# Performance work log

Measured on AMD Instinct MI355X. Metric: run time of the kernel, lower is better.

Reference implementation:

```python
import jax, jax.numpy as jnp
import numpy as np

HID = 512
POOL = 4096
NUM_OBJ = 151
NUM_REL = 51
K = 100
GROUPS = 8
EPS_GN = 1e-5


def _lrga(x, w, b):
    # LowRankAttention: x [N,D] -> [N,2K]
    tmp = jax.nn.relu(x @ w + b)            # [N,4K]
    u, v, z, t = tmp[:, :K], tmp[:, K:2*K], tmp[:, 2*K:3*K], tmp[:, 3*K:]
    # joint_normalize2: scalar 1 / (mean_n(U @ (V^T 1)) + eps)
    norm = u @ jnp.sum(v, axis=0)           # [N]
    d = 1.0 / (jnp.sum(norm) / x.shape[0] + 1e-6)
    res = u @ (v.T @ z)                     # [N,K], low-rank global attention
    return jax.nn.relu(jnp.concatenate((res * d, t), axis=1))


def _group_norm(x, gamma, beta):
    n, c = x.shape
    xg = x.reshape(n, GROUPS, c // GROUPS)
    mu = jnp.mean(xg, axis=-1, keepdims=True)
    var = jnp.var(xg, axis=-1, keepdims=True)
    xn = ((xg - mu) * jax.lax.rsqrt(var + EPS_GN)).reshape(n, c)
    return xn * gamma + beta


def setup_inputs() -> dict:
    key = jax.random.key(0)
    ks = jax.random.split(key, 24)
    n_obj, n_rel = 4096, 16384
    s = 0.02
    inp = {
        'edge_ctx': jax.random.normal(ks[0], (n_obj, HID), jnp.float32),
        'union_features': jax.random.normal(ks[1], (n_rel, POOL), jnp.float32),
        'rel_pair_idxs': jax.random.randint(ks[2], (n_rel, 2), 0, n_obj),
        'obj_preds': jax.random.randint(ks[3], (n_obj,), 0, NUM_OBJ),
        # parameters
        'w_post_emb': jax.random.normal(ks[4], (HID, 2 * HID), jnp.float32) * s,
        'b_post_emb': jnp.zeros((2 * HID,), jnp.float32),
        'w_post_cat': jax.random.normal(ks[5], (2 * HID, POOL), jnp.float32) * s,
        'b_post_cat': jnp.zeros((POOL,), jnp.float32),
        'w_attn1': jax.random.normal(ks[6], (POOL, 4 * K), jnp.float32) * s,
        'b_attn1': jnp.zeros((4 * K,), jnp.float32),
        'w_dr1': jax.random.normal(ks[7], (2 * K + POOL, POOL), jnp.float32) * s,
        'b_dr1': jnp.zeros((POOL,), jnp.float32),
        'gn_gamma': jnp.ones((POOL,), jnp.float32),
        'gn_beta': jnp.zeros((POOL,), jnp.float32),
        'w_attn2': jax.random.normal(ks[8], (POOL, 4 * K), jnp.float32) * s,
        'b_attn2': jnp.zeros((4 * K,), jnp.float32),
        'w_dr2': jax.random.normal(ks[9], (2 * K + POOL, POOL), jnp.float32) * s,
        'b_dr2': jnp.zeros((POOL,), jnp.float32),
        'w_rel': jax.random.normal(ks[10], (POOL, NUM_REL), jnp.float32) * s,
        'b_rel': jnp.zeros((NUM_REL,), jnp.float32),
        'w_ctx': jax.random.normal(ks[11], (2 * HID, NUM_REL), jnp.float32) * s,
        'b_ctx': jnp.zeros((NUM_REL,), jnp.float32),
        'freq_table': jax.random.normal(ks[12], (NUM_OBJ * NUM_OBJ, NUM_REL), jnp.float32) * s,
    }
    return inp


def reference(edge_ctx, union_features, rel_pair_idxs, obj_preds,
              w_post_emb, b_post_emb, w_post_cat, b_post_cat,
              w_attn1, b_attn1, w_dr1, b_dr1, gn_gamma, gn_beta,
              w_attn2, b_attn2, w_dr2, b_dr2,
              w_rel, b_rel, w_ctx, b_ctx, freq_table):
    # post_emb -> split into head/tail halves (view(N,2,H))
    edge_rep = edge_ctx @ w_post_emb + b_post_emb        # [N_obj, 2H]
    head_rep, tail_rep = edge_rep[:, :HID], edge_rep[:, HID:]
    # gather subject/object features per relation pair
    sub, obj = rel_pair_idxs[:, 0], rel_pair_idxs[:, 1]
    prod_rep = jnp.concatenate((head_rep[sub], tail_rep[obj]), axis=-1)  # [N_rel, 2H]
    pair_pred = obj_preds[rel_pair_idxs]                 # [N_rel, 2]
    ctx_gate = prod_rep @ w_post_cat + b_post_cat        # [N_rel, POOL]
    visual_rep = union_features * ctx_gate
    # LRGA block 1
    x_local = jax.nn.relu(visual_rep)                    # dropout = identity (eval)
    x_global = _lrga(union_features, w_attn1, b_attn1)   # [N_rel, 2K]
    x = jnp.concatenate((x_global, x_local), axis=1) @ w_dr1 + b_dr1
    x = _group_norm(jax.nn.relu(x), gn_gamma, gn_beta)
    # LRGA block 2
    x_local = jax.nn.relu(x)
    x_global = _lrga(x, w_attn2, b_attn2)
    visual_rep = jnp.concatenate((x_global, x_local), axis=1) @ w_dr2 + b_dr2
    # fused classification + frequency-bias lookup-add
    rel_dists = visual_rep @ w_rel + b_rel + prod_rep @ w_ctx + b_ctx
    freq = freq_table[pair_pred[:, 0] * NUM_OBJ + pair_pred[:, 1]]
    rel_dists = rel_dists + freq                         # dropout(0.3) = identity (eval)
    return rel_dists
```

## Files before the change

kernel.cpp:

```cpp
#include <hip/hip_runtime.h>

__device__ __forceinline__ short f2bf(float f) {
    unsigned u = __float_as_uint(f);
    unsigned r = (u + 0x7FFFu + ((u >> 16) & 1u)) >> 16;
    return (short)r;
}
__device__ __forceinline__ float bf2f(short s) {
    return __uint_as_float(((unsigned)(unsigned short)s) << 16);
}

typedef short bf16x8 __attribute__((ext_vector_type(8)));
typedef float f32x4  __attribute__((ext_vector_type(4)));

__device__ __forceinline__ void async16(const void* g, void* l) {
    __builtin_amdgcn_global_load_lds(
        (__attribute__((address_space(1))) unsigned int*)(void*)(g),
        (__attribute__((address_space(3))) unsigned int*)(l), 16, 0, 0);
}

#define BAR()    __builtin_amdgcn_s_barrier()
#define SCHED0() __builtin_amdgcn_sched_barrier(0)
#define VMW(n)   asm volatile("s_waitcnt vmcnt(" #n ")" ::: "memory")

template<int MODE>
__global__ __launch_bounds__(256)
void gemm128(const short* __restrict__ A, long lda,
             const short* __restrict__ B,
             const float* __restrict__ bias,
             void* __restrict__ outp, long ldo, int ooff, int nreal,
             const float* __restrict__ gate, short* __restrict__ gate_bf,
             const int* __restrict__ fidx, const float* __restrict__ freq,
             int K)
{
    __shared__ short As[128 * 64];
    __shared__ short Bs[128 * 64];
    const int t = threadIdx.x;
    const int lane = t & 63;
    const int w = t >> 6;
    const long bm = (long)blockIdx.y * 128;
    const long bn = (long)blockIdx.x * 128;

    f32x4 acc[4][4] = {};

    const short* Ab = A + bm * lda;
    const short* Bb = B + bn * (long)K;

    const int wm = (w & 1) * 64, wn = (w >> 1) * 64;
    const int mrow = lane & 15, khi = (lane >> 4) * 8;
    const int swz = mrow & 7;

    for (int k0 = 0; k0 < K; k0 += 64) {
        __syncthreads();
        #pragma unroll
        for (int i = 0; i < 4; ++i) {
            int idx = i * 256 + t;
            int r = idx >> 3, ch = (idx & 7) ^ (r & 7);
            async16(Ab + (long)r * lda + (k0 + ch * 8), &As[idx * 8]);
        }
        #pragma unroll
        for (int i = 0; i < 4; ++i) {
            int idx = i * 256 + t;
            int r = idx >> 3, ch = (idx & 7) ^ (r & 7);
            async16(Bb + (long)r * K + (k0 + ch * 8), &Bs[idx * 8]);
        }
        __syncthreads();

        #pragma unroll
        for (int kk = 0; kk < 64; kk += 32) {
            const int ch = (((kk + khi) >> 3) ^ swz) * 8;
            bf16x8 a[4], b[4];
            #pragma unroll
            for (int im = 0; im < 4; ++im)
                a[im] = *(const bf16x8*)&As[(wm + im * 16 + mrow) * 64 + ch];
            #pragma unroll
            for (int in = 0; in < 4; ++in)
                b[in] = *(const bf16x8*)&Bs[(wn + in * 16 + mrow) * 64 + ch];
            #pragma unroll
            for (int im = 0; im < 4; ++im)
                #pragma unroll
                for (int in = 0; in < 4; ++in)
                    acc[im][in] = __builtin_amdgcn_mfma_f32_16x16x32_bf16(
                        a[im], b[in], acc[im][in], 0, 0, 0);
        }
    }

    const int col = lane & 15, rb = (lane >> 4) * 4;
    #pragma unroll
    for (int in = 0; in < 4; ++in) {
        long n = bn + wn + in * 16 + col;
        if (n >= nreal) continue;
        float bv = bias[n];
        #pragma unroll
        for (int im = 0; im < 4; ++im) {
            #pragma unroll
            for (int r = 0; r < 4; ++r) {
                long m = bm + wm + im * 16 + rb + r;
                float v = acc[im][in][r] + bv;
                if (MODE == 1) v = fmaxf(v, 0.f);
                if (MODE == 2) {
                    float g = gate[m * 4096 + n];
                    gate_bf[m * 4096 + n] = f2bf(g);
                    v = fmaxf(v * g, 0.f);
                }
                if (MODE == 3) {
                    v += freq[(long)fidx[m] * 51 + n];
                    ((float*)outp)[m * 51 + n] = v;
                } else {
                    ((short*)outp)[m * ldo + ooff + n] = f2bf(v);
                }
            }
        }
    }
}

template<int MH>
__device__ __forceinline__ void loadAf(bf16x8 (&a)[4][2], const short* Asb,
                                       int wrow, int fr, int kc0) {
    #pragma unroll
    for (int im = 0; im < 4; ++im) {
        int r = wrow * 128 + MH * 64 + im * 16 + fr;
        const short* rp = Asb + r * 64;
        int s = r & 7;
        a[im][0] = *(const bf16x8*)(rp + ((kc0    ) ^ s) * 8);
        a[im][1] = *(const bf16x8*)(rp + ((kc0 + 4) ^ s) * 8);
    }
}
template<int NH>
__device__ __forceinline__ void loadBf(bf16x8 (&bb)[2][2], const short* Bsb,
                                       int wcol, int fr, int kc0) {
    #pragma unroll
    for (int in = 0; in < 2; ++in) {
        int r = wcol * 64 + NH * 32 + in * 16 + fr;
        const short* rp = Bsb + r * 64;
        int s = r & 7;
        bb[in][0] = *(const bf16x8*)(rp + ((kc0    ) ^ s) * 8);
        bb[in][1] = *(const bf16x8*)(rp + ((kc0 + 4) ^ s) * 8);
    }
}
template<int MH, int NH>
__device__ __forceinline__ void quadf(f32x4 (&acc)[8][4], const bf16x8 (&a)[4][2],
                                      const bf16x8 (&bb)[2][2]) {
    #pragma unroll
    for (int ks = 0; ks < 2; ++ks)
        #pragma unroll
        for (int im = 0; im < 4; ++im)
            #pragma unroll
            for (int in = 0; in < 2; ++in)
                acc[MH * 4 + im][NH * 2 + in] = __builtin_amdgcn_mfma_f32_16x16x32_bf16(
                    a[im][ks], bb[in][ks], acc[MH * 4 + im][NH * 2 + in], 0, 0, 0);
}

template<int MODE>
__global__ __launch_bounds__(512)
void gemm256(const short* __restrict__ A, long lda,
             const short* __restrict__ B,
             const float* __restrict__ bias,
             void* __restrict__ outp, long ldo, int ooff, int nreal,
             const float* __restrict__ gate, short* __restrict__ gate_bf,
             int K)
{
    __shared__ short As[2][256 * 64];
    __shared__ short Bs[2][256 * 64];
    const int t = threadIdx.x;
    const int lane = t & 63;
    const int w = t >> 6;
    const int wrow = w >> 2, wcol = w & 3;

    const int gx = gridDim.x;
    int lin = blockIdx.y * gx + blockIdx.x;
    int q8 = (gx * gridDim.y) >> 3;
    int lin2 = (lin & 7) * q8 + (lin >> 3);
    const long bm = (long)(lin2 / gx) * 256;
    const long bn = (long)(lin2 % gx) * 256;

    const short* Ab = A + bm * lda;
    const short* Bb = B + bn * (long)K;

    const int tq = t >> 3;
    const int scz = (t & 7) ^ (tq & 7);
    const long aoff = (long)tq * lda + scz * 8;
    const int  brw  = (tq >> 5) * 64 + (tq & 31);
    const long boff = (long)brw * K + scz * 8;
    const int  blds = brw * 8 + (t & 7);

    const int fr = lane & 15, kc0 = lane >> 4;

    auto stgA = [&](int buf, int p, long tile) {
        long k0 = tile << 6;
        #pragma unroll
        for (int j = 0; j < 2; ++j) {
            int u = j * 128 + p * 64;
            async16(Ab + (long)u * lda + k0 + aoff, &As[buf][u * 64 + t * 8]);
        }
    };
    auto stgB = [&](int buf, int p, long tile) {
        long k0 = tile << 6;
        #pragma unroll
        for (int j = 0; j < 2; ++j) {
            int u = j * 128 + p * 32;
            async16(Bb + (long)u * K + k0 + boff, &Bs[buf][u * 64 + blds * 8]);
        }
    };

    f32x4 acc[8][4] = {};
    bf16x8 a[4][2], b0[2][2], b1[2][2];

    const int NT = K >> 6, NI = NT >> 1;

    stgA(0, 0, 0); stgB(0, 0, 0); stgA(0, 1, 0); stgB(0, 1, 0);
    stgA(1, 0, 1); stgB(1, 0, 1); stgA(1, 1, 1);
    VMW(6);

    for (int it = 0; it < NI; ++it) {
        const long T0 = 2 * it, T1 = 2 * it + 1;
        const bool m0 = (T0 + 2 < NT), m1 = (T1 + 2 < NT);
        const bool last = (it == NI - 1);
        BAR(); SCHED0();
        stgB(1, 1, T1);
        loadAf<0>(a, As[0], wrow, fr, kc0);
        loadBf<0>(b0, Bs[0], wcol, fr, kc0);
        __builtin_amdgcn_s_setprio(1); quadf<0, 0>(acc, a, b0); __builtin_amdgcn_s_setprio(0);
        BAR(); SCHED0();
        if (m0) stgA(0, 0, T0 + 2);
        loadBf<1>(b1, Bs[0], wcol, fr, kc0);
        __builtin_amdgcn_s_setprio(1); quadf<0, 1>(acc, a, b1); __builtin_amdgcn_s_setprio(0);
        BAR(); SCHED0();
        if (m0) stgB(0, 0, T0 + 2);
        loadAf<1>(a, As[0], wrow, fr, kc0);
        __builtin_amdgcn_s_setprio(1); quadf<1, 0>(acc, a, b0); __builtin_amdgcn_s_setprio(0);
        BAR(); SCHED0();
        if (m0) stgA(0, 1, T0 + 2);
        __builtin_amdgcn_s_setprio(1); quadf<1, 1>(acc, a, b1); __builtin_amdgcn_s_setprio(0);
        if (last) { VMW(0); } else { VMW(6); }
        BAR(); SCHED0();
        if (m0) stgB(0, 1, T0 + 2);
        loadAf<0>(a, As[1], wrow, fr, kc0);
        loadBf<0>(b0, Bs[1], wcol, fr, kc0);
        __builtin_amdgcn_s_setprio(1); quadf<0, 0>(acc, a, b0); __builtin_amdgcn_s_setprio(0);
        BAR(); SCHED0();
        if (m1) stgA(1, 0, T1 + 2);
        loadBf<1>(b1, Bs[1], wcol, fr, kc0);
        __builtin_amdgcn_s_setprio(1); quadf<0, 1>(acc, a, b1); __builtin_amdgcn_s_setprio(0);
        BAR(); SCHED0();
        if (m1) stgB(1, 0, T1 + 2);
        loadAf<1>(a, As[1], wrow, fr, kc0);
        __builtin_amdgcn_s_setprio(1); quadf<1, 0>(acc, a, b0); __builtin_amdgcn_s_setprio(0);
        BAR(); SCHED0();
        if (m1) stgA(1, 1, T1 + 2);
        __builtin_amdgcn_s_setprio(1); quadf<1, 1>(acc, a, b1); __builtin_amdgcn_s_setprio(0);
        if (last) { VMW(0); } else { VMW(6); }
    }

    const int col = lane & 15, rb = (lane >> 4) * 4;
    float bv[4];
    #pragma unroll
    for (int in = 0; in < 4; ++in) {
        long n = bn + wcol * 64 + in * 16 + col;
        bv[in] = (n < nreal) ? bias[n] : 0.f;
    }
    #pragma unroll
    for (int im = 0; im < 8; ++im) {
        #pragma unroll
        for (int r = 0; r < 4; ++r) {
            long m = bm + wrow * 128 + im * 16 + rb + r;
            #pragma unroll
            for (int in = 0; in < 4; ++in) {
                long n = bn + wcol * 64 + in * 16 + col;
                if (n >= nreal) continue;
                float v = acc[im][in][r] + bv[in];
                if (MODE == 1) v = fmaxf(v, 0.f);
                if (MODE == 2) {
                    float g = gate[m * 4096 + n];
                    gate_bf[m * 4096 + n] = f2bf(g);
                    v = fmaxf(v * g, 0.f);
                }
                ((short*)outp)[m * ldo + ooff + n] = f2bf(v);
            }
        }
    }
}

__global__ void cvt_bf16(const float* __restrict__ in, short* __restrict__ out, long n) {
    long i = (long)blockIdx.x * 256 + threadIdx.x;
    if (i < n) out[i] = f2bf(in[i]);
}

__global__ __launch_bounds__(256)
void transpose_pad(const float* __restrict__ in, int R, int C,
                   short* __restrict__ out, int Cp, int Rp)
{
    __shared__ float tile[32][33];
    int tx = threadIdx.x, ty = threadIdx.y;
    int c0 = blockIdx.x * 32, r0 = blockIdx.y * 32;
    #pragma unroll
    for (int j = 0; j < 32; j += 8) {
        int r = r0 + ty + j, c = c0 + tx;
        tile[ty + j][tx] = (r < R && c < C) ? in[(long)r * C + c] : 0.f;
    }
    __syncthreads();
    #pragma unroll
    for (int j = 0; j < 32; j += 8) {
        int oc = c0 + ty + j;
        int orr = r0 + tx;
        out[(long)oc * Rp + orr] = f2bf(tile[tx][ty + j]);
    }
}

__global__ void build_wf(const float* __restrict__ w_rel, const float* __restrict__ b_rel,
                         const float* __restrict__ w_ctx, const float* __restrict__ b_ctx,
                         short* __restrict__ wf, float* __restrict__ biasF)
{
    long i = (long)blockIdx.x * 256 + threadIdx.x;
    if (i < 64) biasF[i] = (i < 51) ? b_rel[i] + b_ctx[i] : 0.f;
    if (i >= 128L * 5120) return;
    int n = (int)(i / 5120), k = (int)(i % 5120);
    float v = 0.f;
    if (n < 51) v = (k < 4096) ? w_rel[(long)k * 51 + n] : w_ctx[(long)(k - 4096) * 51 + n];
    wf[i] = f2bf(v);
}

__global__ void gather_prod(const short* __restrict__ erep, const int* __restrict__ pairs,
                            const int* __restrict__ obj_preds,
                            short* __restrict__ vrcat, int* __restrict__ fidx)
{
    long i = blockIdx.x;
    int t = threadIdx.x;
    int s = pairs[2 * i], o = pairs[2 * i + 1];
    if (t == 0) fidx[i] = obj_preds[s] * 151 + obj_preds[o];
    int c = t * 4;
    long src = (long)(c < 512 ? s : o) * 1024 + c;
    *(uint2*)(vrcat + i * 5120 + 4096 + c) = *(const uint2*)(erep + src);
}

__global__ void colsum200(const short* __restrict__ tmp, float* __restrict__ colsum) {
    int t = threadIdx.x;
    if (t >= 200) return;
    const short* p = tmp + (long)blockIdx.x * 128 * 400 + t;
    float s = 0.f;
    for (int r = 0; r < 128; ++r) s += bf2f(p[(long)r * 400]);
    atomicAdd(&colsum[t], s);
}

__global__ void compute_d(const float* __restrict__ cs, float* __restrict__ dout) {
    int t = threadIdx.x;
    float v = cs[t] * cs[100 + t];
    if (t < 36) v += cs[64 + t] * cs[164 + t];
    #pragma unroll
    for (int m = 32; m >= 1; m >>= 1) v += __shfl_xor(v, m, 64);
    if (t == 0) dout[0] = 1.f / (v / 16384.f + 1e-6f);
}

__global__ __launch_bounds__(256)
void vtz_kern(const short* __restrict__ tmp, float* __restrict__ vtz) {
    __shared__ float vs[64 * 100];
    __shared__ float zs[64 * 100];
    int t = threadIdx.x;
    long r0 = (long)blockIdx.x * 64;
    for (int i = t; i < 64 * 200; i += 256) {
        int r = i / 200, c = i % 200;
        float val = bf2f(tmp[(r0 + r) * 400 + 100 + c]);
        if (c < 100) vs[r * 100 + c] = val; else zs[r * 100 + (c - 100)] = val;
    }
    __syncthreads();
    for (int e = t; e < 10000; e += 256) {
        int k = e / 100, l = e % 100;
        float s = 0.f;
        #pragma unroll 4
        for (int r = 0; r < 64; ++r) s += vs[r * 100 + k] * zs[r * 100 + l];
        atomicAdd(&vtz[e], s);
    }
}

__global__ __launch_bounds__(256)
void res_kern(const short* __restrict__ tmp, const float* __restrict__ vtz,
              const float* __restrict__ dptr, short* __restrict__ xcat)
{
    __shared__ float vt[10000];
    __shared__ float us[32 * 100];
    int t = threadIdx.x;
    long r0 = (long)blockIdx.x * 32;
    for (int i = t; i < 10000; i += 256) vt[i] = vtz[i];
    for (int i = t; i < 3200; i += 256) {
        int r = i / 100, c = i % 100;
        us[i] = bf2f(tmp[(r0 + r) * 400 + c]);
    }
    __syncthreads();
    float d = dptr[0];
    for (int e = t; e < 3200; e += 256) {
        int r = e / 100, c = e % 100;
        float s = 0.f;
        #pragma unroll 4
        for (int k = 0; k < 100; ++k) s += us[r * 100 + k] * vt[k * 100 + c];
        xcat[(r0 + r) * 4352 + c] = f2bf(fmaxf(s * d, 0.f));
    }
    for (int e = t; e < 3200; e += 256) {
        int r = e / 100, c = e % 100;
        xcat[(r0 + r) * 4352 + 100 + c] = tmp[(r0 + r) * 400 + 300 + c];
    }
    for (int e = t; e < 32 * 56; e += 256) {
        int r = e / 56, c = e % 56;
        xcat[(r0 + r) * 4352 + 4296 + c] = 0;
    }
}

__global__ __launch_bounds__(256)
void gn_kern(const short* __restrict__ y, const float* __restrict__ gamma,
             const float* __restrict__ beta,
             short* __restrict__ xgn, short* __restrict__ x2cat)
{
    long row = blockIdx.x;
    int t = threadIdx.x;
    const short* p = y + row * 4096 + t * 16;
    const uint4* q = (const uint4*)p;
    uint4 q0 = q[0], q1 = q[1];
    unsigned u[8] = {q0.x, q0.y, q0.z, q0.w, q1.x, q1.y, q1.z, q1.w};
    float v[16];
    #pragma unroll
    for (int i = 0; i < 8; ++i) {
        v[2 * i]     = __uint_as_float(u[i] << 16);
        v[2 * i + 1] = __uint_as_float(u[i] & 0xFFFF0000u);
    }
    float s1 = 0.f, s2 = 0.f;
    #pragma unroll
    for (int i = 0; i < 16; ++i) { s1 += v[i]; s2 += v[i] * v[i]; }
    #pragma unroll
    for (int m = 1; m < 32; m <<= 1) { s1 += __shfl_xor(s1, m, 32); s2 += __shfl_xor(s2, m, 32); }
    float mu = s1 * (1.f / 512.f);
    float var = fmaxf(s2 * (1.f / 512.f) - mu * mu, 0.f);
    float rs = rsqrtf(var + 1e-5f);
    #pragma unroll
    for (int i = 0; i < 16; ++i) {
        int c = t * 16 + i;
        float val = (v[i] - mu) * rs * gamma[c] + beta[c];
        xgn[row * 4096 + c] = f2bf(val);
        x2cat[row * 4352 + 200 + c] = f2bf(fmaxf(val, 0.f));
    }
}

extern "C" void kernel_launch(void* const* d_in, const int* in_sizes, int n_in,
                              void* d_out, int out_size, void* d_ws, size_t ws_size,
                              hipStream_t stream)
{
    (void)in_sizes; (void)n_in; (void)out_size; (void)ws_size;
    const float* edge_ctx   = (const float*)d_in[0];
    const float* unionf     = (const float*)d_in[1];
    const int*   pairs      = (const int*)d_in[2];
    const int*   obj_preds  = (const int*)d_in[3];
    const float* w_post_emb = (const float*)d_in[4];
    const float* b_post_emb = (const float*)d_in[5];
    const float* w_post_cat = (const float*)d_in[6];
    const float* b_post_cat = (const float*)d_in[7];
    const float* w_attn1    = (const float*)d_in[8];
    const float* b_attn1    = (const float*)d_in[9];
    const float* w_dr1      = (const float*)d_in[10];
    const float* b_dr1      = (const float*)d_in[11];
    const float* gamma      = (const float*)d_in[12];
    const float* beta       = (const float*)d_in[13];
    const float* w_attn2    = (const float*)d_in[14];
    const float* b_attn2    = (const float*)d_in[15];
    const float* w_dr2      = (const float*)d_in[16];
    const float* b_dr2      = (const float*)d_in[17];
    const float* w_rel      = (const float*)d_in[18];
    const float* b_rel      = (const float*)d_in[19];
    const float* w_ctx      = (const float*)d_in[20];
    const float* b_ctx      = (const float*)d_in[21];
    const float* freq       = (const float*)d_in[22];

    char* base = (char*)d_ws;
    size_t off = 0;
    auto alloc = [&](size_t b) -> void* {
        void* p = base + off; off += (b + 255) & ~(size_t)255; return p;
    };
    short* ec_bf  = (short*)alloc(4096L * 512 * 2);
    short* wTpe   = (short*)alloc(1024L * 512 * 2);
    short* erep   = (short*)alloc(4096L * 1024 * 2);
    short* vrcat  = (short*)alloc(16384L * 5120 * 2);
    int*   fidx   = (int*)  alloc(16384L * 4);
    short* ubf    = (short*)alloc(16384L * 4096 * 2);
    short* wTpc   = (short*)alloc(4096L * 1024 * 2);
    short* x1cat  = (short*)alloc(16384L * 4352 * 2);
    short* wTa1   = (short*)alloc(512L * 4096 * 2);
    short* wTa2   = (short*)alloc(512L * 4096 * 2);
    short* tmp    = (short*)alloc(16384L * 400 * 2);
    short* wTd1   = (short*)alloc(4096L * 4352 * 2);
    short* wTd2   = (short*)alloc(4096L * 4352 * 2);
    short* x2cat  = (short*)alloc(16384L * 4352 * 2);
    short* wF     = (short*)alloc(128L * 5120 * 2);
    float* biasF  = (float*)alloc(64 * 4);
    float* colsum = (float*)alloc(400 * 4);
    float* vtz    = (float*)alloc(100 * 100 * 4);
    float* dval   = (float*)alloc(4);

    dim3 tb(32, 8);
    cvt_bf16<<<(4096 * 512 + 255) / 256, 256, 0, stream>>>(edge_ctx, ec_bf, 4096L * 512);
    transpose_pad<<<dim3(1024 / 32, 512 / 32), tb, 0, stream>>>(w_post_emb, 512, 1024, wTpe, 1024, 512);
    transpose_pad<<<dim3(4096 / 32, 1024 / 32), tb, 0, stream>>>(w_post_cat, 1024, 4096, wTpc, 4096, 1024);
    transpose_pad<<<dim3(512 / 32, 4096 / 32), tb, 0, stream>>>(w_attn1, 4096, 400, wTa1, 512, 4096);
    transpose_pad<<<dim3(512 / 32, 4096 / 32), tb, 0, stream>>>(w_attn2, 4096, 400, wTa2, 512, 4096);
    transpose_pad<<<dim3(4096 / 32, 4352 / 32), tb, 0, stream>>>(w_dr1, 4296, 4096, wTd1, 4096, 4352);
    transpose_pad<<<dim3(4096 / 32, 4352 / 32), tb, 0, stream>>>(w_dr2, 4296, 4096, wTd2, 4096, 4352);
    build_wf<<<(128 * 5120 + 255) / 256, 256, 0, stream>>>(w_rel, b_rel, w_ctx, b_ctx, wF, biasF);

    gemm128<0><<<dim3(8, 32), 256, 0, stream>>>(ec_bf, 512, wTpe, b_post_emb,
        erep, 1024, 0, 1024, nullptr, nullptr, nullptr, nullptr, 512);
    gather_prod<<<16384, 256, 0, stream>>>(erep, pairs, obj_preds, vrcat, fidx);

    gemm256<2><<<dim3(16, 64), 512, 0, stream>>>(vrcat + 4096, 5120, wTpc, b_post_cat,
        x1cat, 4352, 200, 4096, unionf, ubf, 1024);

    gemm128<1><<<dim3(4, 128), 256, 0, stream>>>(ubf, 4096, wTa1, b_attn1,
        tmp, 400, 0, 400, nullptr, nullptr, nullptr, nullptr, 4096);
    hipMemsetAsync(colsum, 0, 400 * 4, stream);
    hipMemsetAsync(vtz, 0, 100 * 100 * 4, stream);
    colsum200<<<128, 256, 0, stream>>>(tmp, colsum);
    compute_d<<<1, 64, 0, stream>>>(colsum, dval);
    vtz_kern<<<256, 256, 0, stream>>>(tmp, vtz);
    res_kern<<<512, 256, 0, stream>>>(tmp, vtz, dval, x1cat);

    gemm256<1><<<dim3(16, 64), 512, 0, stream>>>(x1cat, 4352, wTd1, b_dr1,
        ubf, 4096, 0, 4096, nullptr, nullptr, 4352);
    gn_kern<<<16384, 256, 0, stream>>>(ubf, gamma, beta, x1cat, x2cat);

    gemm128<1><<<dim3(4, 128), 256, 0, stream>>>(x1cat, 4096, wTa2, b_attn2,
        tmp, 400, 0, 400, nullptr, nullptr, nullptr, nullptr, 4096);
    hipMemsetAsync(colsum, 0, 400 * 4, stream);
    hipMemsetAsync(vtz, 0, 100 * 100 * 4, stream);
    colsum200<<<128, 256, 0, stream>>>(tmp, colsum);
    compute_d<<<1, 64, 0, stream>>>(colsum, dval);
    vtz_kern<<<256, 256, 0, stream>>>(tmp, vtz);
    res_kern<<<512, 256, 0, stream>>>(tmp, vtz, dval, x2cat);

    gemm256<0><<<dim3(16, 64), 512, 0, stream>>>(x2cat, 4352, wTd2, b_dr2,
        vrcat, 5120, 0, 4096, nullptr, nullptr, 4352);
    gemm128<3><<<dim3(1, 128), 256, 0, stream>>>(vrcat, 5120, wF, biasF,
        d_out, 51, 0, 51, nullptr, nullptr, fidx, freq, 5120);
}
```

Before: 2.772 ms.

## Use inline-asm LDS reads with precomputed addresses and restructure barrier schedule

Replaces compiler-generated LDS fragment loads in the 256-tile GEMM with inline ds_read_b128 that use precomputed swizzled base addresses and immediate offsets, which removes per-load address arithmetic. The main loop is reordered so each phase issues its LDS reads and global prefetch, then waits with a barrier and lgkmcnt(0) before the MFMA cluster, and adds a trailing barrier. This gives explicit control over interleaving in a ping-pong style schedule. The cost is many more barriers per iteration and a dependence on hand-computed offsets staying correct for the LDS layout.

Result: faster. 2.552 ms (-7.9%).

```diff
diff --git a/kernel.cpp b/kernel.cpp
--- a/kernel.cpp
+++ b/kernel.cpp
@@ -18,9 +18,29 @@
         (__attribute__((address_space(3))) unsigned int*)(l), 16, 0, 0);
 }
 
+__device__ __forceinline__ unsigned ldsaddr(const void* p) {
+    return (unsigned)(unsigned long long)
+        (__attribute__((address_space(3))) const void*)p;
+}
+
 #define BAR()    __builtin_amdgcn_s_barrier()
 #define SCHED0() __builtin_amdgcn_sched_barrier(0)
+#define LGKM0()  asm volatile("s_waitcnt lgkmcnt(0)" ::: "memory")
 #define VMW(n)   asm volatile("s_waitcnt vmcnt(" #n ")" ::: "memory")
+#define PRIO1()  __builtin_amdgcn_s_setprio(1)
+#define PRIO0()  __builtin_amdgcn_s_setprio(0)
+
+#define DSR(d, va, off) \
+    asm volatile("ds_read_b128 %0, %1 offset:" off : "=v"(d) : "v"(va))
+
+#define LDA8(o0, o1, o2, o3) do { \
+    DSR(a[0][0], avA0, o0); DSR(a[0][1], avA1, o0); \
+    DSR(a[1][0], avA0, o1); DSR(a[1][1], avA1, o1); \
+    DSR(a[2][0], avA0, o2); DSR(a[2][1], avA1, o2); \
+    DSR(a[3][0], avA0, o3); DSR(a[3][1], avA1, o3); } while (0)
+#define LDB4(bb, o0, o1) do { \
+    DSR(bb[0][0], avB0, o0); DSR(bb[0][1], avB1, o0); \
+    DSR(bb[1][0], avB0, o1); DSR(bb[1][1], avB1, o1); } while (0)
 
 template<int MODE>
 __global__ __launch_bounds__(256)
@@ -113,30 +133,6 @@
     }
 }
 
-template<int MH>
-__device__ __forceinline__ void loadAf(bf16x8 (&a)[4][2], const short* Asb,
-                                       int wrow, int fr, int kc0) {
-    #pragma unroll
-    for (int im = 0; im < 4; ++im) {
-        int r = wrow * 128 + MH * 64 + im * 16 + fr;
-        const short* rp = Asb + r * 64;
-        int s = r & 7;
-        a[im][0] = *(const bf16x8*)(rp + ((kc0    ) ^ s) * 8);
-        a[im][1] = *(const bf16x8*)(rp + ((kc0 + 4) ^ s) * 8);
-    }
-}
-template<int NH>
-__device__ __forceinline__ void loadBf(bf16x8 (&bb)[2][2], const short* Bsb,
-                                       int wcol, int fr, int kc0) {
-    #pragma unroll
-    for (int in = 0; in < 2; ++in) {
-        int r = wcol * 64 + NH * 32 + in * 16 + fr;
-        const short* rp = Bsb + r * 64;
-        int s = r & 7;
-        bb[in][0] = *(const bf16x8*)(rp + ((kc0    ) ^ s) * 8);
-        bb[in][1] = *(const bf16x8*)(rp + ((kc0 + 4) ^ s) * 8);
-    }
-}
 template<int MH, int NH>
 __device__ __forceinline__ void quadf(f32x4 (&acc)[8][4], const bf16x8 (&a)[4][2],
                                       const bf16x8 (&bb)[2][2]) {
@@ -185,6 +181,13 @@
 
     const int fr = lane & 15, kc0 = lane >> 4;
 
+    const unsigned As0 = ldsaddr(&As[0][0]);
+    const unsigned Bs0 = ldsaddr(&Bs[0][0]);
+    const unsigned avA0 = As0 + wrow * 16384 + fr * 128 + (((kc0    ) ^ (fr & 7)) << 4);
+    const unsigned avA1 = As0 + wrow * 16384 + fr * 128 + (((kc0 + 4) ^ (fr & 7)) << 4);
+    const unsigned avB0 = Bs0 + wcol * 8192  + fr * 128 + (((kc0    ) ^ (fr & 7)) << 4);
+    const unsigned avB1 = Bs0 + wcol * 8192  + fr * 128 + (((kc0 + 4) ^ (fr & 7)) << 4);
+
     auto stgA = [&](int buf, int p, long tile) {
         long k0 = tile << 6;
         #pragma unroll
@@ -210,46 +213,56 @@
     stgA(0, 0, 0); stgB(0, 0, 0); stgA(0, 1, 0); stgB(0, 1, 0);
     stgA(1, 0, 1); stgB(1, 0, 1); stgA(1, 1, 1);
     VMW(6);
+    BAR();
 
     for (int it = 0; it < NI; ++it) {
         const long T0 = 2 * it, T1 = 2 * it + 1;
         const bool m0 = (T0 + 2 < NT), m1 = (T1 + 2 < NT);
         const bool last = (it == NI - 1);
-        BAR(); SCHED0();
+        LDA8("0", "2048", "4096", "6144");
+        LDB4(b0, "0", "2048");
         stgB(1, 1, T1);
-        loadAf<0>(a, As[0], wrow, fr, kc0);
-        loadBf<0>(b0, Bs[0], wcol, fr, kc0);
-        __builtin_amdgcn_s_setprio(1); quadf<0, 0>(acc, a, b0); __builtin_amdgcn_s_setprio(0);
-        BAR(); SCHED0();
+        BAR(); LGKM0(); SCHED0();
+        PRIO1(); quadf<0, 0>(acc, a, b0); PRIO0();
+        BAR();
+        LDB4(b1, "4096", "6144");
         if (m0) stgA(0, 0, T0 + 2);
-        loadBf<1>(b1, Bs[0], wcol, fr, kc0);
-        __builtin_amdgcn_s_setprio(1); quadf<0, 1>(acc, a, b1); __builtin_amdgcn_s_setprio(0);
-        BAR(); SCHED0();
+        BAR(); LGKM0(); SCHED0();
+        PRIO1(); quadf<0, 1>(acc, a, b1); PRIO0();
+        BAR();
+        LDA8("8192", "10240", "12288", "14336");
         if (m0) stgB(0, 0, T0 + 2);
-        loadAf<1>(a, As[0], wrow, fr, kc0);
-        __builtin_amdgcn_s_setprio(1); quadf<1, 0>(acc, a, b0); __builtin_amdgcn_s_setprio(0);
-        BAR(); SCHED0();
+        BAR(); LGKM0(); SCHED0();
+        PRIO1(); quadf<1, 0>(acc, a, b0); PRIO0();
+        BAR();
         if (m0) stgA(0, 1, T0 + 2);
-        __builtin_amdgcn_s_setprio(1); quadf<1, 1>(acc, a, b1); __builtin_amdgcn_s_setprio(0);
         if (last) { VMW(0); } else { VMW(6); }
         BAR(); SCHED0();
+        PRIO1(); quadf<1, 1>(acc, a, b1); PRIO0();
+        BAR();
+        LDA8("32768", "34816", "36864", "38912");
+        LDB4(b0, "32768", "34816");
         if (m0) stgB(0, 1, T0 + 2);
-        loadAf<0>(a, As[1], wrow, fr, kc0);
-        loadBf<0>(b0, Bs[1], wcol, fr, kc0);
-        __builtin_amdgcn_s_setprio(1); quadf<0, 0>(acc, a, b0); __builtin_amdgcn_s_setprio(0);
+        BAR(); LGKM0(); SCHED0();
+        PRIO1(); quadf<0, 0>(acc, a, b0); PRIO0();
+        BAR();
+        LDB4(b1, "36864", "38912");
+        if (m1) stgA(1, 0, T1 + 2);
+        BAR(); LGKM0(); SCHED0();
+        PRIO1(); quadf<0, 1>(acc, a, b1); PRIO0();
+        BAR();
+        LDA8("40960", "43008", "45056", "47104");
+        if (m1) stgB(1, 0, T1 + 2);
+        BAR(); LGKM0(); SCHED0();
+        PRIO1(); quadf<1, 0>(acc, a, b0); PRIO0();
+        BAR();
+        if (m1) stgA(1, 1, T1 + 2);
+        if (last) { VMW(0); } else { VMW(6); }
         BAR(); SCHED0();
-        if (m1) stgA(1, 0, T1 + 2);
-        loadBf<1>(b1, Bs[1], wcol, fr, kc0);
-        __builtin_amdgcn_s_setprio(1); quadf<0, 1>(acc, a, b1); __builtin_amdgcn_s_setprio(0);
-        BAR(); SCHED0();
-        if (m1) stgB(1, 0, T1 + 2);
-        loadAf<1>(a, As[1], wrow, fr, kc0);
-        __builtin_amdgcn_s_setprio(1); quadf<1, 0>(acc, a, b0); __builtin_amdgcn_s_setprio(0);
-        BAR(); SCHED0();
-        if (m1) stgA(1, 1, T1 + 2);
-        __builtin_amdgcn_s_setprio(1); quadf<1, 1>(acc, a, b1); __builtin_amdgcn_s_setprio(0);
-        if (last) { VMW(0); } else { VMW(6); }
-    }
+        PRIO1(); quadf<1, 1>(acc, a, b1); PRIO0();
+        BAR();
+    }
+    VMW(0);
 
     const int col = lane & 15, rb = (lane >> 4) * 4;
     float bv[4];
```
